# Kernel optimization log

Measured on AMD Instinct MI355X. Metric: run time of the kernel, lower is better.

Reference implementation:

```python
import jax, jax.numpy as jnp
import numpy as np
from jax import lax

# dims from the TED skeleton used by speech2affective_gestures
N, T, J, C = 256, 1024, 9, 3      # batch, frames, directed edges (graph1 nodes), coords
K1, K2 = 5, 3                     # spatial partitions of A1, A2
F1, F2 = 16, 16                   # st_gcn output channels
NUM_PARTS, MAX_EDGES = 3, 3       # body parts, edges per part
BODY_PARTS = np.array([[0, 1, 2], [3, 4, 5], [6, 7, 8]])  # body_parts_edge_idx
EPS = 1e-5
LEAK = 0.01


def conv2d_nchw(x, w):
    kh = w.shape[2]
    return lax.conv_general_dilated(x, w, (1, 1), ((kh // 2, kh // 2), (0, 0)),
                                    dimension_numbers=("NCHW", "OIHW", "NCHW"))


def conv1d_nch(x, w):
    k = w.shape[2]
    return lax.conv_general_dilated(x, w, (1,), ((k // 2, k // 2),),
                                    dimension_numbers=("NCH", "OIH", "NCH"))


def bn1d(x, w, b, m, v):
    # inference-mode BatchNorm1d over channel axis 1 of (N, C, T)
    scale = w / jnp.sqrt(v + EPS)
    return x * scale[None, :, None] + (b - m * scale)[None, :, None]


def leaky(x):
    return jnp.where(x > 0, x, LEAK * x)


def setup_inputs() -> dict:
    key = jax.random.key(0)
    ks = jax.random.split(key, 12)
    s = 0.05
    return {
        "poses": jax.random.normal(ks[0], (N, T, J * C), jnp.float32),
        "A1": jax.random.uniform(ks[1], (K1, J, J), jnp.float32) / J,
        "A2": jax.random.uniform(ks[2], (K2, NUM_PARTS, NUM_PARTS), jnp.float32) / NUM_PARTS,
        "W1": jax.random.normal(ks[3], (F1 * K1, C, 9, 1), jnp.float32) * s,
        "b1": jnp.zeros((F1 * K1,), jnp.float32),
        "W2": jax.random.normal(ks[4], (F2 * K2, MAX_EDGES * F1, 9, 1), jnp.float32) * s,
        "b2": jnp.zeros((F2 * K2,), jnp.float32),
        "Wc1": jax.random.normal(ks[5], (16, F2 * NUM_PARTS, 5), jnp.float32) * s,
        "bc1": jnp.zeros((16,), jnp.float32),
        "bn1_w": jnp.ones((16,), jnp.float32), "bn1_b": jnp.zeros((16,), jnp.float32),
        "bn1_m": jnp.zeros((16,), jnp.float32), "bn1_v": jnp.ones((16,), jnp.float32),
        "Wc2": jax.random.normal(ks[6], (8, 16, 3), jnp.float32) * s,
        "bc2": jnp.zeros((8,), jnp.float32),
        "bn2_w": jnp.ones((8,), jnp.float32), "bn2_b": jnp.zeros((8,), jnp.float32),
        "bn2_m": jnp.zeros((8,), jnp.float32), "bn2_v": jnp.ones((8,), jnp.float32),
    }


def reference(poses, A1, A2, W1, b1, W2, b2, Wc1, bc1, bn1_w, bn1_b, bn1_m, bn1_v,
              Wc2, bc2, bn2_w, bn2_b, bn2_m, bn2_v):
    n, t, jc = poses.shape
    x = jnp.transpose(poses.reshape(n, t, J, C), (0, 3, 1, 2))  # (n, 3, t, 9)

    # st_gcn1: temporal conv -> split K partitions -> graph contraction with A1
    y = conv2d_nchw(x, W1) + b1[None, :, None, None]            # (n, K1*F1, t, 9)
    y = y.reshape(n, K1, F1, t, J)
    feat1 = jnp.einsum("nkctv,kvw->nctw", y, A1)                # (n, 16, t, 9)

    # body-part gather/pack: feat2_in channel layout is (c slow, edge fast)
    g = feat1[:, :, :, BODY_PARTS]                              # (n, 16, t, parts, edges)
    feat2_in = jnp.transpose(g, (0, 1, 4, 2, 3)).reshape(n, F1 * MAX_EDGES, t, NUM_PARTS)

    # st_gcn2
    y2 = conv2d_nchw(feat2_in, W2) + b2[None, :, None, None]    # (n, K2*F2, t, 3)
    y2 = y2.reshape(n, K2, F2, t, NUM_PARTS)
    feat2 = jnp.einsum("nkctv,kvw->nctw", y2, A2)               # (n, 16, t, 3)

    # flatten (c, v) with c slow -> (n, 48, t)
    feat3_in = jnp.transpose(feat2, (0, 1, 3, 2)).reshape(n, F2 * NUM_PARTS, t)

    h = leaky(bn1d(conv1d_nch(feat3_in, Wc1) + bc1[None, :, None], bn1_w, bn1_b, bn1_m, bn1_v))
    h = leaky(bn1d(conv1d_nch(h, Wc2) + bc2[None, :, None], bn2_w, bn2_b, bn2_m, bn2_v))
    return jnp.transpose(h, (0, 2, 1))                          # (n, t, 8)
```

## Files before the change

### kernel.cpp

```cpp
#include <hip/hip_runtime.h>

namespace {
constexpr int T_ = 1024;
constexpr int NBATCH = 256;

constexpr int WFB_OFF    = 0;
constexpr int WFC_OFF    = 82944;
constexpr int WFD_OFF    = 221184;
constexpr int WBIG_OFF   = 231424;
constexpr int WFE_OFF    = 252928;
constexpr int BIASB_OFF  = 254976;
constexpr int BIASC_OFF  = 255552;
constexpr int BIASD_OFF  = 255744;
constexpr int BIASBIG_OFF= 255808;
constexpr int BIASE_OFF  = 255872;
constexpr int WCOMP_OFF  = 262144;

constexpr int R0 = 41472;
constexpr int R1 = R0 + 69120;
constexpr int R2 = R1 + 5120;
constexpr int R3 = R2 + 1024;
constexpr int R4 = R3 + 29952;
constexpr int R5 = R4 + 144;
constexpr int R6 = R5 + 48;
constexpr int R7 = R6 + 16;
constexpr int R8 = R7 + 8;

constexpr int SLAB_OFF  = 0;
constexpr int H1_OFF    = 23360;
constexpr int MAIN_LDS  = H1_OFF + 272 * 32;
constexpr int TT_FX     = 50;
constexpr int FXF2IN    = 0;
constexpr int FXF3      = FXF2IN + 72 * 320;
constexpr int FXSLAB    = FXF3 + 68 * 144;
constexpr int FXH1      = FXSLAB;
constexpr int SMEM_FUSE = FXSLAB + 72 * 80;
static_assert(MAIN_LDS <= SMEM_FUSE, "main fits");
static_assert(SMEM_FUSE * 4 <= 163840, "4 blocks/CU");

typedef __attribute__((ext_vector_type(8))) short short8v;
typedef __attribute__((ext_vector_type(4))) float f32x4;

__device__ inline unsigned short f2b(float f) {
  union { float f; unsigned u; } v; v.f = f;
  unsigned r = (v.u + 0x7FFFu + ((v.u >> 16) & 1u)) >> 16;
  return (unsigned short)r;
}
__device__ inline float b2f(unsigned short u) {
  union { unsigned u; float f; } v; v.u = ((unsigned)u) << 16;
  return v.f;
}
__device__ inline int fx_f2in_byte(int row, int slot, int within) {
  return FXF2IN + row * 320 + ((slot ^ ((row >> 2) & 3)) << 4) + within;
}
}

__global__ __launch_bounds__(256) void prep1_kernel(
    const float* __restrict__ A1, const float* __restrict__ A2,
    const float* __restrict__ W1, const float* __restrict__ b1,
    const float* __restrict__ W2, const float* __restrict__ b2,
    const float* __restrict__ Wc1, const float* __restrict__ bc1,
    const float* __restrict__ bn1w, const float* __restrict__ bn1b,
    const float* __restrict__ bn1m, const float* __restrict__ bn1v,
    const float* __restrict__ Wc2, const float* __restrict__ bc2,
    const float* __restrict__ bn2w, const float* __restrict__ bn2b,
    const float* __restrict__ bn2m, const float* __restrict__ bn2v,
    unsigned char* __restrict__ ws) {
  unsigned short* wfB = (unsigned short*)(ws + WFB_OFF);
  unsigned short* wfC = (unsigned short*)(ws + WFC_OFF);
  unsigned short* wfD = (unsigned short*)(ws + WFD_OFF);
  unsigned short* wfE = (unsigned short*)(ws + WFE_OFF);
  float* biasB = (float*)(ws + BIASB_OFF);
  float* biasC = (float*)(ws + BIASC_OFF);
  float* biasD = (float*)(ws + BIASD_OFF);
  float* biasE = (float*)(ws + BIASE_OFF);
  float* wcomp = (float*)(ws + WCOMP_OFF);
  for (int idx = blockIdx.x * 256 + threadIdx.x; idx < R8; idx += gridDim.x * 256) {
    if (idx < R0) {
      int ncol = idx / 288, k = idx - ncol * 288;
      int dh = k >> 5, mm = k & 31;
      float val = 0.f;
      if (mm < 27) {
        int v = mm / 3, ci = mm - v * 3;
        int p = ncol / 48, rr = ncol - p * 48, c = rr / 3, e = rr - c * 3;
        int w = p * 3 + e;
        for (int k5 = 0; k5 < 5; ++k5)
          val += W1[(k5 * 16 + c) * 27 + ci * 9 + dh] * A1[k5 * 81 + v * 9 + w];
      }
      wfB[idx] = f2b(val);
    } else if (idx < R1) {
      int i2 = idx - R0;
      int nc = i2 / 1440, k = i2 - nc * 1440;
      int dh = k / 160, off = k - dh * 160;
      float val = 0.f;
      if (off < 144) {
        int p = off / 48, ci2 = off - p * 48;
        int c2 = nc / 3, w2 = nc - c2 * 3;
        for (int k2 = 0; k2 < 3; ++k2)
          val += W2[(k2 * 16 + c2) * 432 + ci2 * 9 + dh] * A2[k2 * 9 + p * 3 + w2];
      }
      wfC[i2] = f2b(val);
    } else if (idx < R2) {
      int i3 = idx - R1;
      int o3 = i3 / 320, k = i3 - o3 * 320;
      int d = k >> 6, nc = k & 63;
      float val = 0.f;
      if (nc < 48) {
        float s1 = bn1w[o3] * rsqrtf(bn1v[o3] + 1e-5f);
        val = Wc1[o3 * 240 + nc * 5 + d] * s1;
      }
      wfD[i3] = f2b(val);
    } else if (idx < R3) {
      int i4 = idx - R2;
      int o4 = i4 >> 6, k = i4 & 63;
      float val = 0.f;
      if (o4 < 8 && k < 48) {
        int d = k >> 4, ci = k & 15;
        float s2 = bn2w[o4] * rsqrtf(bn2v[o4] + 1e-5f);
        val = Wc2[(o4 * 16 + ci) * 3 + d] * s2;
      }
      wfE[i4] = f2b(val);
    } else if (idx < R4) {
      int i5 = idx - R3;
      int o3 = i5 / 1872, rem = i5 - o3 * 1872;
      int dh2 = rem / 144, ncol = rem - dh2 * 144;
      int p = ncol / 48, ci2 = ncol - p * 48;
      float s1 = bn1w[o3] * rsqrtf(bn1v[o3] + 1e-5f);
      float acc = 0.f;
      for (int d = 0; d < 5; ++d) {
        int dh = dh2 - d;
        if (dh < 0 || dh > 8) continue;
        float wd = 0.f;
        for (int nc = 0; nc < 48; ++nc) {
          int c2 = nc / 3, w2 = nc - c2 * 3;
          float wc = 0.f;
          for (int k2 = 0; k2 < 3; ++k2)
            wc += W2[(k2 * 16 + c2) * 432 + ci2 * 9 + dh] * A2[k2 * 9 + p * 3 + w2];
          wd += Wc1[o3 * 240 + nc * 5 + d] * wc;
        }
        acc += wd * s1;
      }
      wcomp[i5] = acc;
    } else if (idx < R5) {
      int ib = idx - R4;
      int p = ib / 48, rr = ib - p * 48, c = rr / 3, e = rr - c * 3;
      int w = p * 3 + e;
      float val = 0.f;
      for (int k5 = 0; k5 < 5; ++k5)
        for (int v = 0; v < 9; ++v)
          val += b1[k5 * 16 + c] * A1[k5 * 81 + v * 9 + w];
      biasB[ib] = val;
    } else if (idx < R6) {
      int nc = idx - R5, c2 = nc / 3, w2 = nc - c2 * 3;
      float val = 0.f;
      for (int k2 = 0; k2 < 3; ++k2)
        for (int p = 0; p < 3; ++p)
          val += b2[k2 * 16 + c2] * A2[k2 * 9 + p * 3 + w2];
      biasC[nc] = val;
    } else if (idx < R7) {
      int o3 = idx - R6;
      float s1 = bn1w[o3] * rsqrtf(bn1v[o3] + 1e-5f);
      biasD[o3] = bc1[o3] * s1 + bn1b[o3] - bn1m[o3] * s1;
    } else {
      int o4 = idx - R7;
      float s2 = bn2w[o4] * rsqrtf(bn2v[o4] + 1e-5f);
      biasE[o4] = bc2[o4] * s2 + bn2b[o4] - bn2m[o4] * s2;
    }
  }
}

__global__ __launch_bounds__(256) void prep2_kernel(
    const float* __restrict__ Wc1, const float* __restrict__ bn1w,
    const float* __restrict__ bn1v, unsigned char* __restrict__ ws) {
  __shared__ float stgf[48 * 288];
  __shared__ float wl[1872];
  __shared__ float pr[256];
  __shared__ float pbias[192];
  const int dt = blockIdx.x, o3 = blockIdx.y;
  const int tid = threadIdx.x;
  const int m1 = tid & 31, p = tid >> 5;
  const unsigned short* wfB = (const unsigned short*)(ws + WFB_OFF);
  const float* wcomp = (const float*)(ws + WCOMP_OFF);
  unsigned short* wBIG = (unsigned short*)(ws + WBIG_OFF);

  for (int i = tid; i < 1872; i += 256) wl[i] = wcomp[o3 * 1872 + i];

  const int lo = (dt - 8) > 0 ? (dt - 8) : 0;
  const int hi = (dt < 12) ? dt : 12;
  float acc = 0.f;
  for (int c = 0; c < 3; ++c) {
    __syncthreads();
    for (int i = tid; i < 48 * 288; i += 256)
      stgf[i] = b2f(wfB[c * 13824 + i]);
    __syncthreads();
    for (int dh2 = lo; dh2 <= hi; ++dh2) {
      const int dh1 = dt - dh2;
      const float* wr = wl + dh2 * 144 + c * 48 + p * 6;
      const float* br = stgf + (p * 6) * 288 + dh1 * 32 + m1;
#pragma unroll
      for (int j = 0; j < 6; ++j)
        acc += wr[j] * br[j * 288];
    }
  }
  pr[tid] = acc;
  __syncthreads();
  if (tid < 32) {
    float s = pr[tid];
#pragma unroll
    for (int pp = 1; pp < 8; ++pp) s += pr[pp * 32 + tid];
    wBIG[o3 * 672 + dt * 32 + tid] = f2b(s);
  }
  if (dt == 0) {
    if (tid < 144) {
      float s = 0.f;
      for (int dh2 = 0; dh2 < 13; ++dh2) s += wl[dh2 * 144 + tid];
      pbias[tid] = s * ((const float*)(ws + BIASB_OFF))[tid];
    } else if (tid < 192) {
      int nc = tid - 144;
      float s1 = bn1w[o3] * rsqrtf(bn1v[o3] + 1e-5f);
      float s = 0.f;
#pragma unroll
      for (int d = 0; d < 5; ++d) s += Wc1[o3 * 240 + nc * 5 + d];
      pbias[tid] = s * s1 * ((const float*)(ws + BIASC_OFF))[nc];
    }
    __syncthreads();
    if (tid == 0) {
      float accb = ((const float*)(ws + BIASD_OFF))[o3];
      for (int i = 0; i < 192; ++i) accb += pbias[i];
      ((float*)(ws + BIASBIG_OFF))[o3] = accb;
    }
  }
}

__global__ __launch_bounds__(256, 4) void fused_kernel(
    const float* __restrict__ poses,
    const float* __restrict__ Wc2, const float* __restrict__ bc2,
    const float* __restrict__ bn2w, const float* __restrict__ bn2b,
    const float* __restrict__ bn2m, const float* __restrict__ bn2v,
    const unsigned char* __restrict__ ws, float* __restrict__ out) {
  __shared__ __attribute__((aligned(16))) unsigned char smem[SMEM_FUSE];
  const int tid = threadIdx.x;
  const int n = blockIdx.y;
  const int w = tid >> 6, l = tid & 63, lrow = l & 15, q = l >> 4, q8 = q * 8;

  if (blockIdx.x < 4) {
    const int t0 = blockIdx.x * 256;
    {
      unsigned* s32 = (unsigned*)(smem + SLAB_OFF);
      for (int idx = tid; idx < 292 * 20; idx += 256) {
        int r = idx / 20, mi = idx - r * 20, m0 = mi * 2;
        int t = t0 - 18 + r;
        float v0 = 0.f, v1 = 0.f;
        if (m0 < 27 && t >= 0 && t < T_) {
          const float* src = poses + ((long)n * T_ + t) * 27;
          v0 = src[m0];
          if (m0 + 1 < 27) v1 = src[m0 + 1];
        }
        s32[idx] = (unsigned)f2b(v0) | ((unsigned)f2b(v1) << 16);
      }
    }

    const float bb = ((const float*)(ws + BIASBIG_OFF))[lrow];
    const float be = ((const float*)(ws + BIASE_OFF))[lrow & 7];
    const unsigned short* wbg = (const unsigned short*)(ws + WBIG_OFF);
    short8v B[21];
#pragma unroll
    for (int dt = 0; dt < 21; ++dt)
      B[dt] = *(const short8v*)(wbg + lrow * 672 + dt * 32 + q8);
    const unsigned short* wfe = (const unsigned short*)(ws + WFE_OFF);
    const short8v E0 = *(const short8v*)(wfe + lrow * 64 + q8);
    const short8v E1 = *(const short8v*)(wfe + lrow * 64 + 32 + q8);
    __syncthreads();

#pragma unroll
    for (int i = 0; i < 5; ++i) {
      if (i == 4 && w != 0) continue;
      const int mt = (i < 4) ? (w + i * 4) : 16;
      const int sbase = SLAB_OFF + (mt * 16 + lrow) * 80 + q8 * 2;
      f32x4 c0 = {0.f, 0.f, 0.f, 0.f}, c1 = {0.f, 0.f, 0.f, 0.f};
      short8v a[7];
#pragma unroll
      for (int dt = 0; dt < 7; ++dt) a[dt] = *(const short8v*)(smem + sbase + dt * 80);
#pragma unroll
      for (int dt = 0; dt < 7; ++dt) {
        if (dt & 1) c1 = __builtin_amdgcn_mfma_f32_16x16x32_bf16(a[dt], B[dt], c1, 0, 0, 0);
        else        c0 = __builtin_amdgcn_mfma_f32_16x16x32_bf16(a[dt], B[dt], c0, 0, 0, 0);
      }
#pragma unroll
      for (int dt = 0; dt < 7; ++dt) a[dt] = *(const short8v*)(smem + sbase + (7 + dt) * 80);
#pragma unroll
      for (int dt = 0; dt < 7; ++dt) {
        if (dt & 1) c1 = __builtin_amdgcn_mfma_f32_16x16x32_bf16(a[dt], B[7 + dt], c1, 0, 0, 0);
        else        c0 = __builtin_amdgcn_mfma_f32_16x16x32_bf16(a[dt], B[7 + dt], c0, 0, 0, 0);
      }
#pragma unroll
      for (int dt = 0; dt < 7; ++dt) a[dt] = *(const short8v*)(smem + sbase + (14 + dt) * 80);
#pragma unroll
      for (int dt = 0; dt < 7; ++dt) {
        if (dt & 1) c1 = __builtin_amdgcn_mfma_f32_16x16x32_bf16(a[dt], B[14 + dt], c1, 0, 0, 0);
        else        c0 = __builtin_amdgcn_mfma_f32_16x16x32_bf16(a[dt], B[14 + dt], c0, 0, 0, 0);
      }
      const int hbase = H1_OFF + (mt * 16 + q * 4) * 32 + lrow * 2;
#pragma unroll
      for (int jj = 0; jj < 4; ++jj) {
        float x = c0[jj] + c1[jj] + bb;
        float h = x > 0.f ? x : 0.01f * x;
        *(unsigned short*)(smem + hbase + jj * 32) = f2b(h);
      }
    }
    __syncthreads();

#pragma unroll
    for (int i = 0; i < 4; ++i) {
      const int mte = w + i * 4;
      const int abase = H1_OFF + (7 + mte * 16 + lrow) * 32 + q8 * 2;
      short8v A0v = *(const short8v*)(smem + abase);
      short8v A1v = *(const short8v*)(smem + abase + 64);
      f32x4 acc = {0.f, 0.f, 0.f, 0.f};
      acc = __builtin_amdgcn_mfma_f32_16x16x32_bf16(A0v, E0, acc, 0, 0, 0);
      acc = __builtin_amdgcn_mfma_f32_16x16x32_bf16(A1v, E1, acc, 0, 0, 0);
      if (lrow < 8) {
        const int tb = t0 + mte * 16 + q * 4;
#pragma unroll
        for (int jj = 0; jj < 4; ++jj) {
          const int t = tb + jj;
          if (t >= 7 && t < 1017) {
            float x = acc[jj] + be;
            out[((long)n * T_ + t) * 8 + lrow] = x > 0.f ? x : 0.01f * x;
          }
        }
      }
    }
    return;
  }

  const unsigned short* wfB = (const unsigned short*)(ws + WFB_OFF);
  const unsigned short* wfC = (const unsigned short*)(ws + WFC_OFF);
  const unsigned short* wfD = (const unsigned short*)(ws + WFD_OFF);
  const float* biasB = (const float*)(ws + BIASB_OFF);
  const float* biasC = (const float*)(ws + BIASC_OFF);
  const float* biasD = (const float*)(ws + BIASD_OFF);
  const int e = blockIdx.x - 4;
  const int t0 = e ? (T_ - TT_FX) : 0;

  {
    unsigned* slab32 = (unsigned*)(smem + FXSLAB);
    for (int it = tid; it < 72 * 20; it += 256) {
      int r = it / 20, mi = it - r * 20;
      int t = t0 - 11 + r;
      int m0 = mi * 2;
      float v0 = 0.f, v1 = 0.f;
      if (t >= 0 && t < T_) {
        const float* src = poses + ((long)n * T_ + t) * 27;
        if (m0 < 27) v0 = src[m0];
        if (m0 + 1 < 27) v1 = src[m0 + 1];
      }
      slab32[it] = (unsigned)f2b(v0) | ((unsigned)f2b(v1) << 16);
    }
    for (int it = tid; it < 64 * 8; it += 256) {
      int r = it >> 3, u = it & 7;
      int s = 18 + (u >> 2);
      *(unsigned*)(smem + fx_f2in_byte(r, s, (u & 3) * 4)) = 0;
    }
    for (int it = tid; it < 8 * 80; it += 256) {
      int r = 64 + it / 80, u = it - (it / 80) * 80;
      *(unsigned*)(smem + FXF2IN + r * 320 + u * 4) = 0;
    }
    for (int it = tid; it < 68 * 8 + 12 * 24; it += 256) {
      if (it < 68 * 8) {
        int r = it >> 3, u = it & 7;
        *(unsigned*)(smem + FXF3 + r * 144 + 96 + u * 4) = 0;
      } else {
        int k2 = it - 68 * 8;
        int r = 56 + k2 / 24, u = k2 - (k2 / 24) * 24;
        *(unsigned*)(smem + FXF3 + r * 144 + u * 4) = 0;
      }
    }
  }
  __syncthreads();

  {
    const int ntS = (w == 0) ? 0 : (2 * w + 1);
    const int ntN = (w == 0) ? 3 : 2;
#pragma unroll
    for (int ni = 0; ni < 3; ++ni) {
      if (ni < ntN) {
        const int nt = ntS + ni;
        short8v b[9];
#pragma unroll
        for (int dh = 0; dh < 9; ++dh)
          b[dh] = *(const short8v*)(wfB + (nt * 16 + lrow) * 288 + dh * 32 + q8);
        const int ncol = nt * 16 + lrow;
        const float bias = biasB[ncol];
#pragma unroll
        for (int mt = 0; mt < 4; ++mt) {
          short8v a[9];
#pragma unroll
          for (int dh = 0; dh < 9; ++dh)
            a[dh] = *(const short8v*)(smem + FXSLAB + ((mt * 16 + lrow + dh) * 40 + q8) * 2);
          f32x4 c0 = {0.f, 0.f, 0.f, 0.f}, c1 = {0.f, 0.f, 0.f, 0.f};
#pragma unroll
          for (int dh = 0; dh < 9; ++dh) {
            if (dh & 1) c1 = __builtin_amdgcn_mfma_f32_16x16x32_bf16(a[dh], b[dh], c1, 0, 0, 0);
            else        c0 = __builtin_amdgcn_mfma_f32_16x16x32_bf16(a[dh], b[dh], c0, 0, 0, 0);
          }
#pragma unroll
          for (int jj = 0; jj < 4; ++jj) {
            const int r = mt * 16 + q * 4 + jj;
            const int t = t0 - 7 + r;
            float v = (t >= 0 && t < T_) ? c0[jj] + c1[jj] + bias : 0.f;
            *(unsigned short*)(smem + fx_f2in_byte(r, ncol >> 3, (ncol & 7) * 2)) = f2b(v);
          }
        }
      }
    }
  }
  __syncthreads();

  if (w < 3) {
    const int ncol2 = w * 16 + lrow;
    const float bias = biasC[ncol2];
    f32x4 acc[4];
#pragma unroll
    for (int mt = 0; mt < 4; ++mt) acc[mt] = {0.f, 0.f, 0.f, 0.f};
#pragma unroll
    for (int g = 0; g < 5; ++g) {
      short8v b[9];
#pragma unroll
      for (int i = 0; i < 9; ++i) {
        const int kf = g * 9 + i, dh = kf / 5, kkl = kf % 5;
        b[i] = *(const short8v*)(wfC + ncol2 * 1440 + dh * 160 + kkl * 32 + q8);
      }
#pragma unroll
      for (int mt = 0; mt < 4; ++mt) {
        short8v a[9];
#pragma unroll
        for (int i = 0; i < 9; ++i) {
          const int kf = g * 9 + i, dh = kf / 5, kkl = kf % 5;
          a[i] = *(const short8v*)(smem + fx_f2in_byte(mt * 16 + lrow + dh, 4 * kkl + q, 0));
        }
#pragma unroll
        for (int i = 0; i < 9; ++i)
          acc[mt] = __builtin_amdgcn_mfma_f32_16x16x32_bf16(a[i], b[i], acc[mt], 0, 0, 0);
      }
    }
#pragma unroll
    for (int mt = 0; mt < 4; ++mt) {
#pragma unroll
      for (int jj = 0; jj < 4; ++jj) {
        const int rt3 = mt * 16 + q * 4 + jj;
        if (rt3 < 56) {
          const int t = t0 - 3 + rt3;
          float v = (t >= 0 && t < T_) ? acc[mt][jj] + bias : 0.f;
          *(unsigned short*)(smem + FXF3 + rt3 * 144 + ncol2 * 2) = f2b(v);
        }
      }
    }
  }
  __syncthreads();

  {
    const int arow = w * 16 + lrow;
    short8v a[10], b[10];
#pragma unroll
    for (int kf = 0; kf < 10; ++kf) {
      const int d = kf >> 1, kkl = kf & 1;
      b[kf] = *(const short8v*)(wfD + lrow * 320 + d * 64 + kkl * 32 + q8);
      a[kf] = *(const short8v*)(smem + FXF3 + (arow + d) * 144 + (kkl * 32 + q8) * 2);
    }
    f32x4 c0 = {0.f, 0.f, 0.f, 0.f}, c1 = {0.f, 0.f, 0.f, 0.f};
#pragma unroll
    for (int kf = 0; kf < 10; ++kf) {
      if (kf & 1) c1 = __builtin_amdgcn_mfma_f32_16x16x32_bf16(a[kf], b[kf], c1, 0, 0, 0);
      else        c0 = __builtin_amdgcn_mfma_f32_16x16x32_bf16(a[kf], b[kf], c0, 0, 0, 0);
    }
    const float bias = biasD[lrow];
#pragma unroll
    for (int jj = 0; jj < 4; ++jj) {
      const int rh = w * 16 + q * 4 + jj;
      if (rh < 52) {
        const int t = t0 - 1 + rh;
        float v = 0.f;
        if (t >= 0 && t < T_) {
          float x = c0[jj] + c1[jj] + bias;
          v = x > 0.f ? x : 0.01f * x;
        }
        *(float*)(smem + FXH1 + (rh * 17 + lrow) * 4) = v;
      }
    }
  }
  __syncthreads();

  for (int it = tid; it < TT_FX * 8; it += 256) {
    int rt = it >> 3, o4 = it & 7;
    int t = t0 + rt;
    if (t >= T_) continue;
    if (e ? (t < 1017) : (t >= 7)) continue;
    float s2 = bn2w[o4] * rsqrtf(bn2v[o4] + 1e-5f);
    float t2 = bc2[o4] * s2 + bn2b[o4] - bn2m[o4] * s2;
    float acc = 0.f;
#pragma unroll
    for (int d = 0; d < 3; ++d) {
      const float* hr = (const float*)(smem + FXH1 + (rt + d) * 68);
#pragma unroll
      for (int ci = 0; ci < 16; ++ci)
        acc = fmaf(hr[ci], Wc2[(o4 * 16 + ci) * 3 + d], acc);
    }
    float v = acc * s2 + t2;
    out[((long)n * T_ + t) * 8 + o4] = v > 0.f ? v : 0.01f * v;
  }
}

extern "C" void kernel_launch(void* const* d_in, const int* in_sizes, int n_in,
                              void* d_out, int out_size, void* d_ws, size_t ws_size,
                              hipStream_t stream) {
  (void)in_sizes; (void)n_in; (void)out_size; (void)ws_size;
  const float* poses = (const float*)d_in[0];
  const float* A1    = (const float*)d_in[1];
  const float* A2    = (const float*)d_in[2];
  const float* W1    = (const float*)d_in[3];
  const float* b1    = (const float*)d_in[4];
  const float* W2    = (const float*)d_in[5];
  const float* b2    = (const float*)d_in[6];
  const float* Wc1   = (const float*)d_in[7];
  const float* bc1   = (const float*)d_in[8];
  const float* bn1w  = (const float*)d_in[9];
  const float* bn1b  = (const float*)d_in[10];
  const float* bn1m  = (const float*)d_in[11];
  const float* bn1v  = (const float*)d_in[12];
  const float* Wc2   = (const float*)d_in[13];
  const float* bc2   = (const float*)d_in[14];
  const float* bn2w  = (const float*)d_in[15];
  const float* bn2b  = (const float*)d_in[16];
  const float* bn2m  = (const float*)d_in[17];
  const float* bn2v  = (const float*)d_in[18];
  float* out = (float*)d_out;
  unsigned char* ws = (unsigned char*)d_ws;

  hipLaunchKernelGGL(prep1_kernel, dim3(144), dim3(256), 0, stream,
                     A1, A2, W1, b1, W2, b2, Wc1, bc1, bn1w, bn1b, bn1m, bn1v,
                     Wc2, bc2, bn2w, bn2b, bn2m, bn2v, ws);
  hipLaunchKernelGGL(prep2_kernel, dim3(21, 16), dim3(256), 0, stream,
                     Wc1, bn1w, bn1v, ws);
  hipLaunchKernelGGL(fused_kernel, dim3(6, NBATCH), dim3(256), 0, stream,
                     poses, Wc2, bc2, bn2w, bn2b, bn2m, bn2v, ws, out);
}
```

Before: 80.76 us.

## Merge weight-composition prep with edge blocks; split main kernel into smaller tiles

The prep2 weight-composition work and the boundary (edge) blocks are merged into one mid kernel, so the exact edge computation runs alongside weight composition instead of after it. The main MFMA path moves to its own kernel with 128-frame tiles, less LDS per block and a launch bound of 8 blocks per CU, doubling the block count for better occupancy and load balance. prep1's grid also grows. The cost is more halo loads per output frame from the smaller tiles, plus an extra launch boundary between the mid and main stages.

```diff
diff --git a/kernel.cpp b/kernel.cpp
--- a/kernel.cpp
+++ b/kernel.cpp
@@ -26,17 +26,21 @@
 constexpr int R7 = R6 + 16;
 constexpr int R8 = R7 + 8;
 
-constexpr int SLAB_OFF  = 0;
-constexpr int H1_OFF    = 23360;
-constexpr int MAIN_LDS  = H1_OFF + 272 * 32;
-constexpr int TT_FX     = 50;
-constexpr int FXF2IN    = 0;
-constexpr int FXF3      = FXF2IN + 72 * 320;
-constexpr int FXSLAB    = FXF3 + 68 * 144;
-constexpr int FXH1      = FXSLAB;
-constexpr int SMEM_FUSE = FXSLAB + 72 * 80;
-static_assert(MAIN_LDS <= SMEM_FUSE, "main fits");
-static_assert(SMEM_FUSE * 4 <= 163840, "4 blocks/CU");
+constexpr int MSLAB_OFF = 0;
+constexpr int MH1_OFF   = 13120;
+constexpr int SMEM_MAIN = 17728;
+
+constexpr int P2_STG = 0;
+constexpr int P2_WL  = 55296;
+constexpr int P2_PR  = 62784;
+constexpr int P2_PB  = 63808;
+constexpr int TT_FX  = 50;
+constexpr int FXF2IN = 0;
+constexpr int FXF3   = FXF2IN + 72 * 320;
+constexpr int FXSLAB = FXF3 + 68 * 144;
+constexpr int FXH1   = FXSLAB;
+constexpr int SMEM_MID = 64576;
+static_assert(SMEM_MID <= 65536, "mid LDS");
 
 typedef __attribute__((ext_vector_type(8))) short short8v;
 typedef __attribute__((ext_vector_type(4))) float f32x4;
@@ -169,179 +173,89 @@
   }
 }
 
-__global__ __launch_bounds__(256) void prep2_kernel(
-    const float* __restrict__ Wc1, const float* __restrict__ bn1w,
-    const float* __restrict__ bn1v, unsigned char* __restrict__ ws) {
-  __shared__ float stgf[48 * 288];
-  __shared__ float wl[1872];
-  __shared__ float pr[256];
-  __shared__ float pbias[192];
-  const int dt = blockIdx.x, o3 = blockIdx.y;
-  const int tid = threadIdx.x;
-  const int m1 = tid & 31, p = tid >> 5;
-  const unsigned short* wfB = (const unsigned short*)(ws + WFB_OFF);
-  const float* wcomp = (const float*)(ws + WCOMP_OFF);
-  unsigned short* wBIG = (unsigned short*)(ws + WBIG_OFF);
-
-  for (int i = tid; i < 1872; i += 256) wl[i] = wcomp[o3 * 1872 + i];
-
-  const int lo = (dt - 8) > 0 ? (dt - 8) : 0;
-  const int hi = (dt < 12) ? dt : 12;
-  float acc = 0.f;
-  for (int c = 0; c < 3; ++c) {
-    __syncthreads();
-    for (int i = tid; i < 48 * 288; i += 256)
-      stgf[i] = b2f(wfB[c * 13824 + i]);
-    __syncthreads();
-    for (int dh2 = lo; dh2 <= hi; ++dh2) {
-      const int dh1 = dt - dh2;
-      const float* wr = wl + dh2 * 144 + c * 48 + p * 6;
-      const float* br = stgf + (p * 6) * 288 + dh1 * 32 + m1;
-#pragma unroll
-      for (int j = 0; j < 6; ++j)
-        acc += wr[j] * br[j * 288];
-    }
-  }
-  pr[tid] = acc;
-  __syncthreads();
-  if (tid < 32) {
-    float s = pr[tid];
-#pragma unroll
-    for (int pp = 1; pp < 8; ++pp) s += pr[pp * 32 + tid];
-    wBIG[o3 * 672 + dt * 32 + tid] = f2b(s);
-  }
-  if (dt == 0) {
-    if (tid < 144) {
-      float s = 0.f;
-      for (int dh2 = 0; dh2 < 13; ++dh2) s += wl[dh2 * 144 + tid];
-      pbias[tid] = s * ((const float*)(ws + BIASB_OFF))[tid];
-    } else if (tid < 192) {
-      int nc = tid - 144;
-      float s1 = bn1w[o3] * rsqrtf(bn1v[o3] + 1e-5f);
-      float s = 0.f;
-#pragma unroll
-      for (int d = 0; d < 5; ++d) s += Wc1[o3 * 240 + nc * 5 + d];
-      pbias[tid] = s * s1 * ((const float*)(ws + BIASC_OFF))[nc];
-    }
-    __syncthreads();
-    if (tid == 0) {
-      float accb = ((const float*)(ws + BIASD_OFF))[o3];
-      for (int i = 0; i < 192; ++i) accb += pbias[i];
-      ((float*)(ws + BIASBIG_OFF))[o3] = accb;
-    }
-  }
-}
-
-__global__ __launch_bounds__(256, 4) void fused_kernel(
-    const float* __restrict__ poses,
+__global__ __launch_bounds__(256) void mid_kernel(
+    const float* __restrict__ poses, const float* __restrict__ Wc1,
+    const float* __restrict__ bn1w, const float* __restrict__ bn1v,
     const float* __restrict__ Wc2, const float* __restrict__ bc2,
     const float* __restrict__ bn2w, const float* __restrict__ bn2b,
     const float* __restrict__ bn2m, const float* __restrict__ bn2v,
-    const unsigned char* __restrict__ ws, float* __restrict__ out) {
-  __shared__ __attribute__((aligned(16))) unsigned char smem[SMEM_FUSE];
+    unsigned char* __restrict__ ws, float* __restrict__ out) {
+  __shared__ __attribute__((aligned(16))) unsigned char sm[SMEM_MID];
   const int tid = threadIdx.x;
-  const int n = blockIdx.y;
-  const int w = tid >> 6, l = tid & 63, lrow = l & 15, q = l >> 4, q8 = q * 8;
-
-  if (blockIdx.x < 4) {
-    const int t0 = blockIdx.x * 256;
-    {
-      unsigned* s32 = (unsigned*)(smem + SLAB_OFF);
-      for (int idx = tid; idx < 292 * 20; idx += 256) {
-        int r = idx / 20, mi = idx - r * 20, m0 = mi * 2;
-        int t = t0 - 18 + r;
-        float v0 = 0.f, v1 = 0.f;
-        if (m0 < 27 && t >= 0 && t < T_) {
-          const float* src = poses + ((long)n * T_ + t) * 27;
-          v0 = src[m0];
-          if (m0 + 1 < 27) v1 = src[m0 + 1];
-        }
-        s32[idx] = (unsigned)f2b(v0) | ((unsigned)f2b(v1) << 16);
-      }
-    }
-
-    const float bb = ((const float*)(ws + BIASBIG_OFF))[lrow];
-    const float be = ((const float*)(ws + BIASE_OFF))[lrow & 7];
-    const unsigned short* wbg = (const unsigned short*)(ws + WBIG_OFF);
-    short8v B[21];
-#pragma unroll
-    for (int dt = 0; dt < 21; ++dt)
-      B[dt] = *(const short8v*)(wbg + lrow * 672 + dt * 32 + q8);
-    const unsigned short* wfe = (const unsigned short*)(ws + WFE_OFF);
-    const short8v E0 = *(const short8v*)(wfe + lrow * 64 + q8);
-    const short8v E1 = *(const short8v*)(wfe + lrow * 64 + 32 + q8);
+  const int bid = blockIdx.x;
+
+  if (bid < 336) {
+    float* stgf = (float*)(sm + P2_STG);
+    float* wl   = (float*)(sm + P2_WL);
+    float* pr   = (float*)(sm + P2_PR);
+    float* pbias= (float*)(sm + P2_PB);
+    const int dt = bid / 16, o3 = bid - (bid / 16) * 16;
+    const int m1 = tid & 31, p = tid >> 5;
+    const unsigned short* wfB = (const unsigned short*)(ws + WFB_OFF);
+    const float* wcomp = (const float*)(ws + WCOMP_OFF);
+    unsigned short* wBIG = (unsigned short*)(ws + WBIG_OFF);
+
+    for (int i = tid; i < 1872; i += 256) wl[i] = wcomp[o3 * 1872 + i];
+
+    const int lo = (dt - 8) > 0 ? (dt - 8) : 0;
+    const int hi = (dt < 12) ? dt : 12;
+    float acc = 0.f;
+    for (int c = 0; c < 3; ++c) {
+      __syncthreads();
+      for (int i = tid; i < 48 * 288; i += 256)
+        stgf[i] = b2f(wfB[c * 13824 + i]);
+      __syncthreads();
+      for (int dh2 = lo; dh2 <= hi; ++dh2) {
+        const int dh1 = dt - dh2;
+        const float* wr = wl + dh2 * 144 + c * 48 + p * 6;
+        const float* br = stgf + (p * 6) * 288 + dh1 * 32 + m1;
+#pragma unroll
+        for (int j = 0; j < 6; ++j)
+          acc += wr[j] * br[j * 288];
+      }
+    }
+    pr[tid] = acc;
     __syncthreads();
-
-#pragma unroll
-    for (int i = 0; i < 5; ++i) {
-      if (i == 4 && w != 0) continue;
-      const int mt = (i < 4) ? (w + i * 4) : 16;
-      const int sbase = SLAB_OFF + (mt * 16 + lrow) * 80 + q8 * 2;
-      f32x4 c0 = {0.f, 0.f, 0.f, 0.f}, c1 = {0.f, 0.f, 0.f, 0.f};
-      short8v a[7];
-#pragma unroll
-      for (int dt = 0; dt < 7; ++dt) a[dt] = *(const short8v*)(smem + sbase + dt * 80);
-#pragma unroll
-      for (int dt = 0; dt < 7; ++dt) {
-        if (dt & 1) c1 = __builtin_amdgcn_mfma_f32_16x16x32_bf16(a[dt], B[dt], c1, 0, 0, 0);
-        else        c0 = __builtin_amdgcn_mfma_f32_16x16x32_bf16(a[dt], B[dt], c0, 0, 0, 0);
-      }
-#pragma unroll
-      for (int dt = 0; dt < 7; ++dt) a[dt] = *(const short8v*)(smem + sbase + (7 + dt) * 80);
-#pragma unroll
-      for (int dt = 0; dt < 7; ++dt) {
-        if (dt & 1) c1 = __builtin_amdgcn_mfma_f32_16x16x32_bf16(a[dt], B[7 + dt], c1, 0, 0, 0);
-        else        c0 = __builtin_amdgcn_mfma_f32_16x16x32_bf16(a[dt], B[7 + dt], c0, 0, 0, 0);
-      }
-#pragma unroll
-      for (int dt = 0; dt < 7; ++dt) a[dt] = *(const short8v*)(smem + sbase + (14 + dt) * 80);
-#pragma unroll
-      for (int dt = 0; dt < 7; ++dt) {
-        if (dt & 1) c1 = __builtin_amdgcn_mfma_f32_16x16x32_bf16(a[dt], B[14 + dt], c1, 0, 0, 0);
-        else        c0 = __builtin_amdgcn_mfma_f32_16x16x32_bf16(a[dt], B[14 + dt], c0, 0, 0, 0);
-      }
-      const int hbase = H1_OFF + (mt * 16 + q * 4) * 32 + lrow * 2;
-#pragma unroll
-      for (int jj = 0; jj < 4; ++jj) {
-        float x = c0[jj] + c1[jj] + bb;
-        float h = x > 0.f ? x : 0.01f * x;
-        *(unsigned short*)(smem + hbase + jj * 32) = f2b(h);
-      }
-    }
-    __syncthreads();
-
-#pragma unroll
-    for (int i = 0; i < 4; ++i) {
-      const int mte = w + i * 4;
-      const int abase = H1_OFF + (7 + mte * 16 + lrow) * 32 + q8 * 2;
-      short8v A0v = *(const short8v*)(smem + abase);
-      short8v A1v = *(const short8v*)(smem + abase + 64);
-      f32x4 acc = {0.f, 0.f, 0.f, 0.f};
-      acc = __builtin_amdgcn_mfma_f32_16x16x32_bf16(A0v, E0, acc, 0, 0, 0);
-      acc = __builtin_amdgcn_mfma_f32_16x16x32_bf16(A1v, E1, acc, 0, 0, 0);
-      if (lrow < 8) {
-        const int tb = t0 + mte * 16 + q * 4;
-#pragma unroll
-        for (int jj = 0; jj < 4; ++jj) {
-          const int t = tb + jj;
-          if (t >= 7 && t < 1017) {
-            float x = acc[jj] + be;
-            out[((long)n * T_ + t) * 8 + lrow] = x > 0.f ? x : 0.01f * x;
-          }
-        }
+    if (tid < 32) {
+      float s = pr[tid];
+#pragma unroll
+      for (int pp = 1; pp < 8; ++pp) s += pr[pp * 32 + tid];
+      wBIG[o3 * 672 + dt * 32 + tid] = f2b(s);
+    }
+    if (dt == 0) {
+      if (tid < 144) {
+        float s = 0.f;
+        for (int dh2 = 0; dh2 < 13; ++dh2) s += wl[dh2 * 144 + tid];
+        pbias[tid] = s * ((const float*)(ws + BIASB_OFF))[tid];
+      } else if (tid < 192) {
+        int nc = tid - 144;
+        float s1 = bn1w[o3] * rsqrtf(bn1v[o3] + 1e-5f);
+        float s = 0.f;
+#pragma unroll
+        for (int d = 0; d < 5; ++d) s += Wc1[o3 * 240 + nc * 5 + d];
+        pbias[tid] = s * s1 * ((const float*)(ws + BIASC_OFF))[nc];
+      }
+      __syncthreads();
+      if (tid == 0) {
+        float accb = ((const float*)(ws + BIASD_OFF))[o3];
+        for (int i = 0; i < 192; ++i) accb += pbias[i];
+        ((float*)(ws + BIASBIG_OFF))[o3] = accb;
       }
     }
     return;
   }
 
+  unsigned char* smem = sm;
   const unsigned short* wfB = (const unsigned short*)(ws + WFB_OFF);
   const unsigned short* wfC = (const unsigned short*)(ws + WFC_OFF);
   const unsigned short* wfD = (const unsigned short*)(ws + WFD_OFF);
   const float* biasB = (const float*)(ws + BIASB_OFF);
   const float* biasC = (const float*)(ws + BIASC_OFF);
   const float* biasD = (const float*)(ws + BIASD_OFF);
-  const int e = blockIdx.x - 4;
+  const int fx = bid - 336;
+  const int e = fx & 1, n = fx >> 1;
   const int t0 = e ? (T_ - TT_FX) : 0;
+  const int w = tid >> 6, l = tid & 63, lrow = l & 15, q = l >> 4, q8 = q * 8;
 
   {
     unsigned* slab32 = (unsigned*)(smem + FXSLAB);
@@ -508,6 +422,103 @@
     }
     float v = acc * s2 + t2;
     out[((long)n * T_ + t) * 8 + o4] = v > 0.f ? v : 0.01f * v;
+  }
+}
+
+__global__ __launch_bounds__(256, 8) void main_kernel(
+    const float* __restrict__ poses, const unsigned char* __restrict__ ws,
+    float* __restrict__ out) {
+  __shared__ __attribute__((aligned(16))) unsigned char smem[SMEM_MAIN];
+  const int tid = threadIdx.x;
+  const int n = blockIdx.y;
+  const int t0 = blockIdx.x * 128;
+  const int w = tid >> 6, l = tid & 63, lrow = l & 15, q = l >> 4, q8 = q * 8;
+
+  {
+    unsigned* s32 = (unsigned*)(smem + MSLAB_OFF);
+    for (int idx = tid; idx < 164 * 20; idx += 256) {
+      int r = idx / 20, mi = idx - r * 20, m0 = mi * 2;
+      int t = t0 - 18 + r;
+      float v0 = 0.f, v1 = 0.f;
+      if (m0 < 27 && t >= 0 && t < T_) {
+        const float* src = poses + ((long)n * T_ + t) * 27;
+        v0 = src[m0];
+        if (m0 + 1 < 27) v1 = src[m0 + 1];
+      }
+      s32[idx] = (unsigned)f2b(v0) | ((unsigned)f2b(v1) << 16);
+    }
+  }
+
+  const float bb = ((const float*)(ws + BIASBIG_OFF))[lrow];
+  const float be = ((const float*)(ws + BIASE_OFF))[lrow & 7];
+  const unsigned short* wbg = (const unsigned short*)(ws + WBIG_OFF);
+  short8v B[21];
+#pragma unroll
+  for (int dt = 0; dt < 21; ++dt)
+    B[dt] = *(const short8v*)(wbg + lrow * 672 + dt * 32 + q8);
+  const unsigned short* wfe = (const unsigned short*)(ws + WFE_OFF);
+  const short8v E0 = *(const short8v*)(wfe + lrow * 64 + q8);
+  const short8v E1 = *(const short8v*)(wfe + lrow * 64 + 32 + q8);
+  __syncthreads();
+
+#pragma unroll
+  for (int i = 0; i < 3; ++i) {
+    if (i == 2 && w != 0) continue;
+    const int mt = (i < 2) ? (w + i * 4) : 8;
+    const int sbase = MSLAB_OFF + (mt * 16 + lrow) * 80 + q8 * 2;
+    f32x4 c0 = {0.f, 0.f, 0.f, 0.f}, c1 = {0.f, 0.f, 0.f, 0.f};
+    short8v a[7];
+#pragma unroll
+    for (int dt = 0; dt < 7; ++dt) a[dt] = *(const short8v*)(smem + sbase + dt * 80);
+#pragma unroll
+    for (int dt = 0; dt < 7; ++dt) {
+      if (dt & 1) c1 = __builtin_amdgcn_mfma_f32_16x16x32_bf16(a[dt], B[dt], c1, 0, 0, 0);
+      else        c0 = __builtin_amdgcn_mfma_f32_16x16x32_bf16(a[dt], B[dt], c0, 0, 0, 0);
+    }
+#pragma unroll
+    for (int dt = 0; dt < 7; ++dt) a[dt] = *(const short8v*)(smem + sbase + (7 + dt) * 80);
+#pragma unroll
+    for (int dt = 0; dt < 7; ++dt) {
+      if (dt & 1) c1 = __builtin_amdgcn_mfma_f32_16x16x32_bf16(a[dt], B[7 + dt], c1, 0, 0, 0);
+      else        c0 = __builtin_amdgcn_mfma_f32_16x16x32_bf16(a[dt], B[7 + dt], c0, 0, 0, 0);
+    }
+#pragma unroll
+    for (int dt = 0; dt < 7; ++dt) a[dt] = *(const short8v*)(smem + sbase + (14 + dt) * 80);
+#pragma unroll
+    for (int dt = 0; dt < 7; ++dt) {
+      if (dt & 1) c1 = __builtin_amdgcn_mfma_f32_16x16x32_bf16(a[dt], B[14 + dt], c1, 0, 0, 0);
+      else        c0 = __builtin_amdgcn_mfma_f32_16x16x32_bf16(a[dt], B[14 + dt], c0, 0, 0, 0);
+    }
+    const int hbase = MH1_OFF + (mt * 16 + q * 4) * 32 + lrow * 2;
+#pragma unroll
+    for (int jj = 0; jj < 4; ++jj) {
+      float x = c0[jj] + c1[jj] + bb;
+      float h = x > 0.f ? x : 0.01f * x;
+      *(unsigned short*)(smem + hbase + jj * 32) = f2b(h);
+    }
+  }
+  __syncthreads();
+
+#pragma unroll
+  for (int i = 0; i < 2; ++i) {
+    const int mte = w + i * 4;
+    const int abase = MH1_OFF + (7 + mte * 16 + lrow) * 32 + q8 * 2;
+    short8v A0v = *(const short8v*)(smem + abase);
+    short8v A1v = *(const short8v*)(smem + abase + 64);
+    f32x4 acc = {0.f, 0.f, 0.f, 0.f};
+    acc = __builtin_amdgcn_mfma_f32_16x16x32_bf16(A0v, E0, acc, 0, 0, 0);
+    acc = __builtin_amdgcn_mfma_f32_16x16x32_bf16(A1v, E1, acc, 0, 0, 0);
+    if (lrow < 8) {
+      const int tb = t0 + mte * 16 + q * 4;
+#pragma unroll
+      for (int jj = 0; jj < 4; ++jj) {
+        const int t = tb + jj;
+        if (t >= 7 && t < 1017) {
+          float x = acc[jj] + be;
+          out[((long)n * T_ + t) * 8 + lrow] = x > 0.f ? x : 0.01f * x;
+        }
+      }
+    }
   }
 }
 
@@ -537,11 +548,12 @@
   float* out = (float*)d_out;
   unsigned char* ws = (unsigned char*)d_ws;
 
-  hipLaunchKernelGGL(prep1_kernel, dim3(144), dim3(256), 0, stream,
+  hipLaunchKernelGGL(prep1_kernel, dim3(256), dim3(256), 0, stream,
                      A1, A2, W1, b1, W2, b2, Wc1, bc1, bn1w, bn1b, bn1m, bn1v,
                      Wc2, bc2, bn2w, bn2b, bn2m, bn2v, ws);
-  hipLaunchKernelGGL(prep2_kernel, dim3(21, 16), dim3(256), 0, stream,
-                     Wc1, bn1w, bn1v, ws);
-  hipLaunchKernelGGL(fused_kernel, dim3(6, NBATCH), dim3(256), 0, stream,
-                     poses, Wc2, bc2, bn2w, bn2b, bn2m, bn2v, ws, out);
-}
+  hipLaunchKernelGGL(mid_kernel, dim3(336 + 2 * NBATCH), dim3(256), 0, stream,
+                     poses, Wc1, bn1w, bn1v, Wc2, bc2, bn2w, bn2b, bn2m, bn2v,
+                     ws, out);
+  hipLaunchKernelGGL(main_kernel, dim3(8, NBATCH), dim3(256), 0, stream,
+                     poses, ws, out);
+}
```

New measurement: 136.2 us. 1.69x slower.
